# Kernel optimization log

Measured on AMD Instinct MI355X. Metric: run time of the kernel, lower is better.

## Reference

```python
import jax, jax.numpy as jnp
import numpy as np

# Static CT geometry (ctlib-style): parallel-beam pixel-driven backprojection
VIEWS, DETS = 512, 512   # sinogram: angles x detector bins
H, W = 256, 256          # reconstructed image grid


def setup_inputs() -> dict:
    key = jax.random.key(0)
    proj = jax.random.normal(key, (4, 1, VIEWS, DETS), dtype=jnp.float32)
    # options = [dImg (pixel size), dDet (detector bin size), Ang0, dAng]
    options = jnp.array([1.0, 1.5, 0.0, np.pi / VIEWS], dtype=jnp.float32)
    return {"proj": proj, "options": options}


def reference(proj, options):
    # proj: [B, 1, VIEWS, DETS] sinogram; returns image [B, 1, H, W]
    dImg, dDet, ang0, dAng = options[0], options[1], options[2], options[3]

    ang = ang0 + dAng * jnp.arange(VIEWS, dtype=jnp.float32)          # [V]
    cos_a, sin_a = jnp.cos(ang), jnp.sin(ang)
    # pixel-center world coordinates (y axis points up)
    xs = (jnp.arange(W, dtype=jnp.float32) - (W - 1) / 2.0) * dImg     # [W]
    ys = ((H - 1) / 2.0 - jnp.arange(H, dtype=jnp.float32)) * dImg     # [H]

    # signed distance of each pixel to the detector axis for each view: t[v,y,x]
    t = cos_a[:, None, None] * xs[None, None, :] + sin_a[:, None, None] * ys[None, :, None]
    u = t / dDet + (DETS - 1) / 2.0                                    # fractional detector coord

    i0 = jnp.floor(u)
    w = u - i0                                                         # linear interp weight
    i0i = i0.astype(jnp.int32)
    i1i = i0i + 1
    m0 = ((i0i >= 0) & (i0i < DETS)).astype(proj.dtype)
    m1 = ((i1i >= 0) & (i1i < DETS)).astype(proj.dtype)
    i0c = jnp.clip(i0i, 0, DETS - 1)
    i1c = jnp.clip(i1i, 0, DETS - 1)

    p = proj[:, 0]                                                     # [B, V, D]
    vix = jnp.arange(VIEWS)[:, None, None]                             # [V,1,1]
    p0 = p[:, vix, i0c]                                                # [B, V, H, W]
    p1 = p[:, vix, i1c]
    val = p0 * ((1.0 - w) * m0) + p1 * (w * m1)                        # interpolated ray values

    img = dAng * jnp.sum(val, axis=1)                                  # accumulate over views
    return img[:, None, :, :]
```

## Files before the change

### kernel.cpp

```cpp
#include <hip/hip_runtime.h>
#include <math.h>

#define VIEWS  512
#define DETS   512
#define HH     256
#define WW     256
#define VSPLIT 8
#define VCHUNK (VIEWS / VSPLIT)
#define TS     32
#define CV     16
#define WIN    48
#define NCHUNK (VCHUNK / CV)

__global__ __launch_bounds__(256, 8) void backproj_kernel(
    const float* __restrict__ proj,
    const float* __restrict__ options,
    float* __restrict__ out)
{
    __shared__ float2 s_cs[VCHUNK];
    __shared__ float4 s_pk[2][CV];
    __shared__ float  s_win[2][CV][WIN];

    const float dImg = options[0];
    const float dDet = options[1];
    const float ang0 = options[2];
    const float dAng = options[3];

    const int tid = threadIdx.x;
    const int blk = blockIdx.x;
    const int vq  = blk & 7;
    const int tx  = (blk >> 3) & 7;
    const int ty  = (blk >> 6) & 7;
    const int b   = blk >> 9;
    const int v0  = vq * VCHUNK;
    const int x0t = tx * TS;
    const int y0t = ty * TS;

    if (tid < VCHUNK) {
        float a = ang0 + dAng * (float)(v0 + tid);
        float ss, cc;
        sincosf(a, &ss, &cc);
        s_cs[tid] = make_float2(cc, ss);
    }

    const float sc   = dImg / dDet;
    const float uoff = (DETS - 1) * 0.5f;

    const int xl = tid & 31;
    const int yg = tid >> 5;
    const float xs = ((float)(x0t + xl) - (WW - 1) * 0.5f) * sc;
    float ys[4];
#pragma unroll
    for (int k = 0; k < 4; ++k)
        ys[k] = ((HH - 1) * 0.5f - (float)(y0t + yg * 4 + k)) * sc;

    const float xa = ((float)x0t - (WW - 1) * 0.5f) * sc;
    const float xb = ((float)(x0t + TS - 1) - (WW - 1) * 0.5f) * sc;
    const float ya = ((HH - 1) * 0.5f - (float)y0t) * sc;
    const float yb = ((HH - 1) * 0.5f - (float)(y0t + TS - 1)) * sc;

    const int sv = tid >> 4;
    const int sj = tid & 15;
    const float* __restrict__ pbase = proj + (size_t)(b * VIEWS + v0) * DETS;

    __syncthreads();

    float t0, t1, t2, cR, sR, w0f;
    {
        float2 cs = s_cs[sv];
        cR = cs.x; sR = cs.y;
        float umin = fminf(cR * xa, cR * xb) + fminf(sR * ya, sR * yb) + uoff;
        w0f = floorf(umin) - 2.0f;
        const float* row = pbase + (size_t)sv * DETS + (int)w0f;
        t0 = row[sj]; t1 = row[sj + 16]; t2 = row[sj + 32];
    }
    s_win[0][sv][sj]      = t0;
    s_win[0][sv][sj + 16] = t1;
    s_win[0][sv][sj + 32] = t2;
    if (sj == 0) s_pk[0][sv] = make_float4(cR, sR, uoff - w0f, 0.0f);
    __syncthreads();

    float acc[4] = {0.f, 0.f, 0.f, 0.f};

    for (int ch = 0; ch < NCHUNK; ++ch) {
        const int cur = ch & 1;
        const int nxt = cur ^ 1;

        if (ch + 1 < NCHUNK) {
            int gv = (ch + 1) * CV + sv;
            float2 cs = s_cs[gv];
            cR = cs.x; sR = cs.y;
            float umin = fminf(cR * xa, cR * xb) + fminf(sR * ya, sR * yb) + uoff;
            w0f = floorf(umin) - 2.0f;
            const float* row = pbase + (size_t)gv * DETS + (int)w0f;
            t0 = row[sj]; t1 = row[sj + 16]; t2 = row[sj + 32];
        }

#pragma unroll 4
        for (int vv = 0; vv < CV; ++vv) {
            float4 pk = s_pk[cur][vv];
            float tb  = fmaf(pk.x, xs, pk.z);
            const float* win = s_win[cur][vv];
#pragma unroll
            for (int k = 0; k < 4; ++k) {
                float u = fmaf(pk.y, ys[k], tb);
                int   i = (int)u;
                float w = __builtin_amdgcn_fractf(u);
                float p0 = win[i];
                float p1 = win[i + 1];
                acc[k] = fmaf(w, p1 - p0, acc[k] + p0);
            }
        }

        if (ch + 1 < NCHUNK) {
            s_win[nxt][sv][sj]      = t0;
            s_win[nxt][sv][sj + 16] = t1;
            s_win[nxt][sv][sj + 32] = t2;
            if (sj == 0) s_pk[nxt][sv] = make_float4(cR, sR, uoff - w0f, 0.0f);
            __syncthreads();
        }
    }

    float* o = out + ((size_t)b * HH + (y0t + yg * 4)) * WW + x0t + xl;
#pragma unroll
    for (int k = 0; k < 4; ++k)
        atomicAdd(o + (size_t)k * WW, acc[k] * dAng);
}

extern "C" void kernel_launch(void* const* d_in, const int* in_sizes, int n_in,
                              void* d_out, int out_size, void* d_ws, size_t ws_size,
                              hipStream_t stream) {
    const float* proj    = (const float*)d_in[0];
    const float* options = (const float*)d_in[1];
    float* out = (float*)d_out;

    hipMemsetAsync(d_out, 0, (size_t)out_size * sizeof(float), stream);

    dim3 grid(4 * 64 * VSPLIT);
    dim3 block(256);
    backproj_kernel<<<grid, block, 0, stream>>>(proj, options, out);
}
```

Baseline: 85.47 us.

## Share four LDS window loads across the four pixel rows via clamped piecewise interpolation

The four vertically adjacent pixels a thread handles map to detector coordinates spanning under three bins. The inner loop now loads four consecutive window samples once per view instead of eight. Each pixel's linear interpolation is rebuilt as a sum of clamped weights times the neighbouring differences, plus a shared base term. This cuts LDS reads and address arithmetic but adds several min/max and FMA operations per pixel, and it relies on the per-view span staying within three bins.

```diff
diff --git a/kernel.cpp b/kernel.cpp
--- a/kernel.cpp
+++ b/kernel.cpp
@@ -48,11 +48,9 @@
 
     const int xl = tid & 31;
     const int yg = tid >> 5;
-    const float xs = ((float)(x0t + xl) - (WW - 1) * 0.5f) * sc;
-    float ys[4];
-#pragma unroll
-    for (int k = 0; k < 4; ++k)
-        ys[k] = ((HH - 1) * 0.5f - (float)(y0t + yg * 4 + k)) * sc;
+    const float xs  = ((float)(x0t + xl) - (WW - 1) * 0.5f) * sc;
+    const float ys0 = ((HH - 1) * 0.5f - (float)(y0t + yg * 4)) * sc;
+    const float ys3 = ys0 - 3.0f * sc;
 
     const float xa = ((float)x0t - (WW - 1) * 0.5f) * sc;
     const float xb = ((float)(x0t + TS - 1) - (WW - 1) * 0.5f) * sc;
@@ -65,22 +63,23 @@
 
     __syncthreads();
 
-    float t0, t1, t2, cR, sR, w0f;
+    float t0, t1, t2, cR, sR, w0f, dR;
     {
         float2 cs = s_cs[sv];
         cR = cs.x; sR = cs.y;
         float umin = fminf(cR * xa, cR * xb) + fminf(sR * ya, sR * yb) + uoff;
         w0f = floorf(umin) - 2.0f;
+        dR  = sR * sc;
         const float* row = pbase + (size_t)sv * DETS + (int)w0f;
         t0 = row[sj]; t1 = row[sj + 16]; t2 = row[sj + 32];
     }
     s_win[0][sv][sj]      = t0;
     s_win[0][sv][sj + 16] = t1;
     s_win[0][sv][sj + 32] = t2;
-    if (sj == 0) s_pk[0][sv] = make_float4(cR, sR, uoff - w0f, 0.0f);
+    if (sj == 0) s_pk[0][sv] = make_float4(cR, sR, uoff - w0f, dR);
     __syncthreads();
 
-    float acc[4] = {0.f, 0.f, 0.f, 0.f};
+    float acc0 = 0.f, acc1 = 0.f, acc2 = 0.f, acc3 = 0.f, accq = 0.f;
 
     for (int ch = 0; ch < NCHUNK; ++ch) {
         const int cur = ch & 1;
@@ -92,6 +91,7 @@
             cR = cs.x; sR = cs.y;
             float umin = fminf(cR * xa, cR * xb) + fminf(sR * ya, sR * yb) + uoff;
             w0f = floorf(umin) - 2.0f;
+            dR  = sR * sc;
             const float* row = pbase + (size_t)gv * DETS + (int)w0f;
             t0 = row[sj]; t1 = row[sj + 16]; t2 = row[sj + 32];
         }
@@ -100,15 +100,45 @@
         for (int vv = 0; vv < CV; ++vv) {
             float4 pk = s_pk[cur][vv];
             float tb  = fmaf(pk.x, xs, pk.z);
+            float u0  = fmaf(pk.y, ys0, tb);
+            float u3  = fmaf(pk.y, ys3, tb);
+            float mF  = floorf(fminf(u0, u3));
+            int   mi  = (int)mF;
             const float* win = s_win[cur][vv];
-#pragma unroll
-            for (int k = 0; k < 4; ++k) {
-                float u = fmaf(pk.y, ys[k], tb);
-                int   i = (int)u;
-                float w = __builtin_amdgcn_fractf(u);
-                float p0 = win[i];
-                float p1 = win[i + 1];
-                acc[k] = fmaf(w, p1 - p0, acc[k] + p0);
+            float q0 = win[mi];
+            float q1 = win[mi + 1];
+            float q2 = win[mi + 2];
+            float q3 = win[mi + 3];
+            float d0 = q1 - q0, d1 = q2 - q1, d2 = q3 - q2;
+            float f0 = u0 - mF;
+            float f3 = u3 - mF;
+            float dd = pk.w;
+            float f1 = f0 - dd;
+            float f2 = f3 + dd;
+            accq += q0;
+            {
+                float c0 = fminf(f0, 1.0f);
+                float c1 = fminf(fmaxf(f0 - 1.0f, 0.0f), 1.0f);
+                float c2 = fminf(fmaxf(f0 - 2.0f, 0.0f), 1.0f);
+                acc0 = fmaf(c0, d0, acc0); acc0 = fmaf(c1, d1, acc0); acc0 = fmaf(c2, d2, acc0);
+            }
+            {
+                float c0 = fminf(f1, 1.0f);
+                float c1 = fminf(fmaxf(f1 - 1.0f, 0.0f), 1.0f);
+                float c2 = fminf(fmaxf(f1 - 2.0f, 0.0f), 1.0f);
+                acc1 = fmaf(c0, d0, acc1); acc1 = fmaf(c1, d1, acc1); acc1 = fmaf(c2, d2, acc1);
+            }
+            {
+                float c0 = fminf(f2, 1.0f);
+                float c1 = fminf(fmaxf(f2 - 1.0f, 0.0f), 1.0f);
+                float c2 = fminf(fmaxf(f2 - 2.0f, 0.0f), 1.0f);
+                acc2 = fmaf(c0, d0, acc2); acc2 = fmaf(c1, d1, acc2); acc2 = fmaf(c2, d2, acc2);
+            }
+            {
+                float c0 = fminf(f3, 1.0f);
+                float c1 = fminf(fmaxf(f3 - 1.0f, 0.0f), 1.0f);
+                float c2 = fminf(fmaxf(f3 - 2.0f, 0.0f), 1.0f);
+                acc3 = fmaf(c0, d0, acc3); acc3 = fmaf(c1, d1, acc3); acc3 = fmaf(c2, d2, acc3);
             }
         }
 
@@ -116,15 +146,16 @@
             s_win[nxt][sv][sj]      = t0;
             s_win[nxt][sv][sj + 16] = t1;
             s_win[nxt][sv][sj + 32] = t2;
-            if (sj == 0) s_pk[nxt][sv] = make_float4(cR, sR, uoff - w0f, 0.0f);
+            if (sj == 0) s_pk[nxt][sv] = make_float4(cR, sR, uoff - w0f, dR);
             __syncthreads();
         }
     }
 
     float* o = out + ((size_t)b * HH + (y0t + yg * 4)) * WW + x0t + xl;
-#pragma unroll
-    for (int k = 0; k < 4; ++k)
-        atomicAdd(o + (size_t)k * WW, acc[k] * dAng);
+    atomicAdd(o,                  (acc0 + accq) * dAng);
+    atomicAdd(o + WW,             (acc1 + accq) * dAng);
+    atomicAdd(o + 2 * (size_t)WW, (acc2 + accq) * dAng);
+    atomicAdd(o + 3 * (size_t)WW, (acc3 + accq) * dAng);
 }
 
 extern "C" void kernel_launch(void* const* d_in, const int* in_sizes, int n_in,
```

Measured after the change: 87.71 us. +2.6%, slower.
